# Kernel optimization log

Measured on AMD Instinct MI355X. Metric: run time of the kernel, lower is better.

## Reference

```python
import jax, jax.numpy as jnp
import numpy as np

N = 8192
NUM_CLASSES = 5
DIM = 3
EPS = 15.0
MIN_POINTS = 5
N_BATCH = 2


def setup_inputs() -> dict:
    key = jax.random.key(0)
    k1, k2, k3, k4 = jax.random.split(key, 4)
    # coords in a 96^3 box so eps=15 neighborhoods contain > minPoints same-group points
    coords = jax.random.uniform(k1, (N, DIM)) * 96.0
    batch = jax.random.randint(k2, (N, 1), 0, N_BATCH).astype(jnp.float32)
    feat = jax.random.normal(k3, (N, 1))
    seg = jax.random.normal(k4, (N, NUM_CLASSES))
    x = jnp.concatenate([coords, batch, feat, seg], axis=1).astype(jnp.float32)
    return {"x": x}


def _dbscan_labels(x):
    """Per-point DBSCAN cluster labels, run independently per (batch, class) group.
    noise = -1; cluster ids start at 0 within each group, ordered by the smallest
    point index of each cluster's core component (matches the serial scan order
    of the original implementation). Border points get the smallest adjacent
    cluster id (= first cluster to reach them in the serial algorithm)."""
    data = x[:, :-NUM_CLASSES]                 # (N, dim+2)
    seg = x[:, -NUM_CLASSES:]                  # (N, C)
    cls = jnp.argmax(seg, axis=1).astype(jnp.int32)
    b = data[:, DIM].astype(jnp.int32)
    pts = data[:, :DIM]                        # (N, 3)
    group = b * NUM_CLASSES + cls              # (N,) group id per point

    # pairwise squared distances via gram trick; d < eps  <=>  d2 < eps^2
    p2 = jnp.sum(pts * pts, axis=1)
    d2 = p2[:, None] + p2[None, :] - 2.0 * (pts @ pts.T)
    same = group[:, None] == group[None, :]
    adj = same & (d2 < EPS * EPS)              # includes self (d2 ~ 0)
    core = jnp.sum(adj, axis=1) >= MIN_POINTS  # region_query counts self too
    adjcc = adj & core[:, None] & core[None, :]

    idx = jnp.arange(N, dtype=jnp.int32)
    SENT = jnp.int32(N)
    lab0 = jnp.where(core, idx, SENT)

    # connected components of core-core graph via min-label propagation + pointer jumping
    def cond(st):
        return st[1]

    def body(st):
        lab, _ = st
        m = jnp.min(jnp.where(adjcc, lab[None, :], SENT), axis=1)
        nl = jnp.minimum(lab, m)
        safe = jnp.where(core, nl, 0)          # nl < N for core points
        nl2 = jnp.where(core, jnp.minimum(nl, nl[safe]), SENT)
        return (nl2, jnp.any(nl2 != lab))

    rep, _ = jax.lax.while_loop(cond, body, (lab0, jnp.array(True)))

    # per-group sequential cluster ids, ordered by component representative index
    is_rep = core & (rep == idx)
    cid_of_rep = jnp.zeros((N,), jnp.int32)
    for g in range(N_BATCH * NUM_CLASSES):     # fixed small count of groups
        mg = is_rep & (group == g)
        cum = jnp.cumsum(mg.astype(jnp.int32))
        cid_of_rep = jnp.where(mg, cum - 1, cid_of_rep)
    core_cid = cid_of_rep[jnp.where(core, rep, 0)]

    # border points: min cluster id among adjacent core points (same group via adj)
    nb_core = adj & core[None, :]
    BIG = jnp.int32(2 ** 30)
    bcid = jnp.min(jnp.where(nb_core, core_cid[None, :], BIG), axis=1)
    has_core_nb = jnp.any(nb_core, axis=1)
    labels = jnp.where(core, core_cid, jnp.where(has_core_nb, bcid, -1))
    return labels


def reference(x):
    labels = _dbscan_labels(x)
    data = x[:, :-NUM_CLASSES]
    # fixed-shape equivalent of the cluster gather: clustered points keep their
    # data columns (the differentiable part of the original output), noise zeroed
    clustered = jnp.where(labels[:, None] >= 0, data, 0.0)
    return labels, clustered
```

## Files before the change

### kernel.cpp

```cpp
#include <hip/hip_runtime.h>
#include <cstdint>
#include <cstddef>

#define NPTS 8192
#define NWORDS 128
#define XCOLS 10
#define MIN_PTS 5
#define NGROUPS 10
#define BIGC 0x3fffffff

#define NLCAP 1536
#define NSLICE 24
#define ECAP_S 2048
#define EACAP 8192
#define PT 1024
#define PWV 16
#define GT 1024
#define GWV 16

__global__ void __launch_bounds__(PT) k_pairs(
        const float* __restrict__ x, unsigned int* __restrict__ eAll,
        int* __restrict__ ecnt, unsigned long long* __restrict__ corebm_g,
        int* __restrict__ nlist_g, int* __restrict__ nn_g) {
    __shared__ float4 pts[NLCAP];
    __shared__ unsigned long long masks[NWORDS];
    __shared__ int pref[NWORDS];
    __shared__ int srowdeg[64];
    __shared__ int scnt, nnS;

    const int g = blockIdx.x / NSLICE;
    const int s = blockIdx.x % NSLICE;
    const int tid = threadIdx.x, lane = tid & 63, wv = tid >> 6;

    for (int k = tid; k < NLCAP; k += PT)
        pts[k] = make_float4(0.f, 0.f, 0.f, 1.0e38f);
    if (tid < 64) srowdeg[tid] = 0;
    if (tid == 0) scnt = 0;

    for (int w = wv; w < NWORDS; w += PWV) {
        int i = w * 64 + lane;
        const float2* r2 = (const float2*)(x + (size_t)i * XCOLS);
        float2 c23 = r2[1];
        float2 c45 = r2[2];
        float2 c67 = r2[3];
        float2 c89 = r2[4];
        float best = c45.y; int bc = 0;
        if (c67.x > best) { best = c67.x; bc = 1; }
        if (c67.y > best) { best = c67.y; bc = 2; }
        if (c89.x > best) { best = c89.x; bc = 3; }
        if (c89.y > best) { best = c89.y; bc = 4; }
        unsigned long long bm = __ballot((int)c23.y * 5 + bc == g);
        if (lane == 0) masks[w] = bm;
    }
    __syncthreads();
    if (wv == 0) {
        int v0 = __popcll(masks[lane]);
        int incl = v0;
        #pragma unroll
        for (int st = 1; st < 64; st <<= 1) {
            int o = __shfl_up(incl, st);
            if (lane >= st) incl += o;
        }
        pref[lane] = incl - v0;
        int tot0 = __shfl(incl, 63);
        int v1 = __popcll(masks[64 + lane]);
        int incl1 = v1;
        #pragma unroll
        for (int st = 1; st < 64; st <<= 1) {
            int o = __shfl_up(incl1, st);
            if (lane >= st) incl1 += o;
        }
        pref[64 + lane] = tot0 + incl1 - v1;
        if (lane == 63) nnS = tot0 + incl1;
    }
    __syncthreads();
    for (int w = wv; w < NWORDS; w += PWV) {
        unsigned long long bm = masks[w];
        if ((bm >> lane) & 1ull) {
            int p = pref[w] + __popcll(bm & ((1ull << lane) - 1ull));
            if (p < NLCAP) {
                int i = w * 64 + lane;
                const float2* r2 = (const float2*)(x + (size_t)i * XCOLS);
                float2 c01 = r2[0]; float2 c23 = r2[1];
                float px = c01.x, py = c01.y, pz = c23.x;
                pts[p] = make_float4(px, py, pz,
                                     0.5f * (px*px + py*py + pz*pz) - 56.25f);
                if (s == 0) nlist_g[g * NLCAP + p] = i;
            }
        }
    }
    if (s == 0 && tid == 0) nn_g[g] = (nnS > NLCAP) ? NLCAP : nnS;
    __syncthreads();
    const int NN = (nnS > NLCAP) ? NLCAP : nnS;

    const int rrow = s + NSLICE * lane;
    const float4 qu = pts[rrow];
    int rdeg = 0;
    const int NC = (NN + 31) >> 5;
    unsigned int* eg = eAll + (size_t)(g * NSLICE + s) * ECAP_S;
    for (int c = wv; c < NC; c += PWV) {
        int base = c << 5;
        unsigned int bits = 0u;
        #pragma unroll
        for (int t = 0; t < 32; t++) {
            float4 qv = pts[base + t];
            float dt = qu.x*qv.x + qu.y*qv.y + qu.z*qv.z;
            bits |= (dt > qu.w + qv.w) ? (1u << t) : 0u;
        }
        rdeg += __popc(bits);
        int d = rrow - base;
        if (d >= 31) bits = 0u;
        else if (d >= 0) bits &= ~((2u << d) - 1u);
        int cnt = __popc(bits);
        int incl = cnt;
        #pragma unroll
        for (int st = 1; st < 64; st <<= 1) {
            int o = __shfl_up(incl, st);
            if (lane >= st) incl += o;
        }
        int tot = __shfl(incl, 63);
        if (tot > 0) {
            int rb = 0;
            if (lane == 63) rb = atomicAdd(&scnt, tot);
            rb = __shfl(rb, 63);
            unsigned int p = (unsigned int)(rb + incl - cnt);
            unsigned int b = bits;
            unsigned int uhi = (unsigned int)rrow << 11;
            while (b) {
                int t = __ffs(b) - 1; b &= b - 1;
                if (p < ECAP_S) eg[p] = uhi | (unsigned int)(base + t);
                p++;
            }
        }
    }
    if (rdeg > 0) atomicAdd(&srowdeg[lane], rdeg);
    __syncthreads();
    if (wv == 0) {
        unsigned long long cb = __ballot(srowdeg[lane] >= MIN_PTS);
        if (lane == 0) {
            corebm_g[g * NSLICE + s] = cb;
            ecnt[g * NSLICE + s] = (scnt > ECAP_S) ? ECAP_S : scnt;
        }
    }
}

__global__ void __launch_bounds__(GT) k_graph(
        const unsigned int* __restrict__ eAll, const int* __restrict__ ecnt,
        const unsigned long long* __restrict__ corebm_g,
        const int* __restrict__ nlist_g, const int* __restrict__ nn_g,
        const float* __restrict__ x, float* __restrict__ out) {
    __shared__ unsigned int eA[EACAP];
    __shared__ int spar[NLCAP];
    __shared__ int scid[NLCAP];
    __shared__ int scid2[NLCAP];
    __shared__ int sbmin[NLCAP];
    __shared__ int nlist[NLCAP];
    __shared__ unsigned long long cbm[NSLICE];
    __shared__ unsigned long long corelin[NLCAP/64];
    __shared__ unsigned long long repbm[NLCAP/64];
    __shared__ int pref24[NLCAP/64];
    __shared__ int offs[NSLICE], cnts[NSLICE];
    __shared__ int NAs;

    const int g = blockIdx.x;
    const int tid = threadIdx.x, lane = tid & 63, wv = tid >> 6;
    const int NN = nn_g[g];
    volatile int* vpar = spar;

    if (wv == 0) {
        int c = 0;
        if (lane < NSLICE) {
            c = ecnt[g * NSLICE + lane];
            c = (c > ECAP_S) ? ECAP_S : c;
            cbm[lane] = corebm_g[g * NSLICE + lane];
        }
        int incl = c;
        #pragma unroll
        for (int st = 1; st < 32; st <<= 1) {
            int o = __shfl_up(incl, st);
            if (lane >= st) incl += o;
        }
        if (lane < NSLICE) { offs[lane] = incl - c; cnts[lane] = c; }
        if (lane == NSLICE - 1) NAs = incl;
    }
    for (int k = tid; k < NLCAP; k += GT) {
        spar[k] = k;
        sbmin[k] = BIGC;
        nlist[k] = nlist_g[g * NLCAP + k];
    }
    __syncthreads();
    const int NA = (NAs > EACAP) ? EACAP : NAs;
    for (int s2 = wv; s2 < NSLICE; s2 += GWV) {
        const unsigned int* eg = eAll + (size_t)(g * NSLICE + s2) * ECAP_S;
        int off = offs[s2], cn = cnts[s2];
        for (int o = lane; o < cn; o += 64) {
            int dst = off + o;
            if (dst < EACAP) eA[dst] = eg[o];
        }
    }
    for (int w = wv; w < NLCAP / 64; w += GWV) {
        int l = w * 64 + lane;
        bool b = (cbm[l % NSLICE] >> (l / NSLICE)) & 1ull;
        unsigned long long bm = __ballot(b);
        if (lane == 0) corelin[w] = bm;
    }
    __syncthreads();
    auto corebit = [&](int l) -> bool { return (corelin[l >> 6] >> (l & 63)) & 1ull; };
    auto findrep = [&](int v) -> int {
        int curr = vpar[v];
        if (curr != v) {
            int prev = v, next;
            while (curr > (next = vpar[curr])) {
                vpar[prev] = next;
                prev = curr;
                curr = next;
            }
        }
        return curr;
    };

    for (int e = tid; e < NA; e += GT) {
        unsigned int pk = eA[e];
        int u = (int)(pk >> 11), v = (int)(pk & 2047u);
        if (!(corebit(u) && corebit(v))) continue;
        int ru = findrep(u), rv = findrep(v);
        bool repeat;
        do {
            repeat = false;
            if (ru != rv) {
                int lo = (ru < rv) ? ru : rv;
                int hi = (ru < rv) ? rv : ru;
                int ret = atomicCAS(&spar[hi], hi, lo);
                if (ret != hi && ret != lo) { ru = ret; rv = lo; repeat = true; }
            }
        } while (repeat);
    }
    __syncthreads();
    for (int k = tid; k < NN; k += GT)
        spar[k] = findrep(k);
    __syncthreads();
    for (int w = wv; w < NLCAP / 64; w += GWV) {
        int l = w * 64 + lane;
        bool isr = (l < NN) && corebit(l) && (spar[l] == l);
        unsigned long long bm = __ballot(isr);
        if (lane == 0) repbm[w] = bm;
    }
    __syncthreads();
    if (wv == 0 && lane < NLCAP / 64) {
        int c = __popcll(repbm[lane]);
        int incl = c;
        #pragma unroll
        for (int st = 1; st < 32; st <<= 1) {
            int o = __shfl_up(incl, st);
            if (lane >= st) incl += o;
        }
        pref24[lane] = incl - c;
    }
    __syncthreads();
    for (int w = wv; w < NLCAP / 64; w += GWV) {
        int l = w * 64 + lane;
        unsigned long long bm = repbm[w];
        if ((bm >> lane) & 1ull)
            scid[l] = pref24[w] + __popcll(bm & ((1ull << lane) - 1ull));
    }
    __syncthreads();
    for (int k = tid; k < NLCAP; k += GT)
        scid2[k] = (k < NN && corebit(k)) ? scid[spar[k]] : BIGC;
    __syncthreads();
    for (int e = tid; e < NA; e += GT) {
        unsigned int pk = eA[e];
        int u = (int)(pk >> 11), v = (int)(pk & 2047u);
        bool cu = corebit(u), cv = corebit(v);
        if (cu == cv) continue;
        if (cu) atomicMin(&sbmin[v], scid2[u]);
        else    atomicMin(&sbmin[u], scid2[v]);
    }
    __syncthreads();
    for (int k = tid; k < NN; k += GT) {
        int i = nlist[k];
        int c = scid2[k];
        int lbl = (c != BIGC) ? c : ((sbmin[k] < BIGC) ? sbmin[k] : -1);
        out[i] = (float)lbl;
        const float* r = x + (size_t)i * XCOLS;
        float* o = out + NPTS + (size_t)i * 5;
        bool keep = lbl >= 0;
        #pragma unroll
        for (int c5 = 0; c5 < 5; c5++) o[c5] = keep ? r[c5] : 0.0f;
    }
}

extern "C" void kernel_launch(void* const* d_in, const int* in_sizes, int n_in,
                              void* d_out, int out_size, void* d_ws, size_t ws_size,
                              hipStream_t stream) {
    const float* x = (const float*)d_in[0];
    float* out = (float*)d_out;
    char* ws = (char*)d_ws;

    unsigned int* eAll       = (unsigned int*)(ws);
    int* ecnt                = (int*)(ws + 1966080);
    unsigned long long* cbm  = (unsigned long long*)(ws + 1967104);
    int* nlist_g             = (int*)(ws + 1969024);
    int* nn_g                = (int*)(ws + 2030464);

    k_pairs<<<NGROUPS * NSLICE, PT, 0, stream>>>(x, eAll, ecnt, cbm, nlist_g, nn_g);
    k_graph<<<NGROUPS, GT, 0, stream>>>(eAll, ecnt, cbm, nlist_g, nn_g, x, out);
}
```

Before: 81.00 us.

## Fuse pair and graph kernels into one launch with flag-based inter-block handoff

Merges the neighbour-pair kernel and the union-find graph kernel into a single launch. The graph blocks spin on per-slice release/acquire flags, written as a value and its complement, instead of waiting on a kernel boundary. Edge output offsets now come from a buffered two-pass per-wave prefix sum instead of a shared atomic counter. The representative-ID scan is also collapsed into a single-wave sequential pass. This removes a launch gap and atomic contention, but adds spin-waiting blocks and a dependence on co-residency. Flags persist across calls in the workspace, so stale values could be accepted before the current data is written.

```diff
diff --git a/kernel.cpp b/kernel.cpp
--- a/kernel.cpp
+++ b/kernel.cpp
@@ -13,31 +13,43 @@
 #define NSLICE 24
 #define ECAP_S 2048
 #define EACAP 8192
-#define PT 1024
-#define PWV 16
-#define GT 1024
-#define GWV 16
-
-__global__ void __launch_bounds__(PT) k_pairs(
-        const float* __restrict__ x, unsigned int* __restrict__ eAll,
-        int* __restrict__ ecnt, unsigned long long* __restrict__ corebm_g,
-        int* __restrict__ nlist_g, int* __restrict__ nn_g) {
-    __shared__ float4 pts[NLCAP];
-    __shared__ unsigned long long masks[NWORDS];
-    __shared__ int pref[NWORDS];
-    __shared__ int srowdeg[64];
-    __shared__ int scnt, nnS;
-
-    const int g = blockIdx.x / NSLICE;
-    const int s = blockIdx.x % NSLICE;
+#define NCMAX (NLCAP / 32)
+#define NT 1024
+#define NWV 16
+
+struct SmemP {
+    float4 pts[NLCAP];
+    unsigned long long masks[NWORDS];
+    int pref[NWORDS];
+    unsigned int bitsbuf[NCMAX * 64];
+    int wave_tot[NWV], wave_off[NWV];
+    int srowdeg[64];
+    int nnS, totE;
+};
+struct SmemG {
+    unsigned int eA[EACAP];
+    int spar[NLCAP];
+    int scid[NLCAP];
+    int scid2[NLCAP];
+    int sbmin[NLCAP];
+    int nlist[NLCAP];
+    unsigned long long cbm[NSLICE];
+    unsigned long long corelin[NLCAP / 64];
+    int offs[NSLICE], cnts[NSLICE];
+    int NAs;
+};
+
+__device__ __forceinline__ void do_pairs(const float* __restrict__ x, int g, int s,
+        SmemP& sm, unsigned int* __restrict__ eAll, unsigned int* __restrict__ flags,
+        unsigned long long* __restrict__ corebm_g, int* __restrict__ nlist_g,
+        int* __restrict__ nn_g) {
     const int tid = threadIdx.x, lane = tid & 63, wv = tid >> 6;
 
-    for (int k = tid; k < NLCAP; k += PT)
-        pts[k] = make_float4(0.f, 0.f, 0.f, 1.0e38f);
-    if (tid < 64) srowdeg[tid] = 0;
-    if (tid == 0) scnt = 0;
-
-    for (int w = wv; w < NWORDS; w += PWV) {
+    for (int k = tid; k < NLCAP; k += NT)
+        sm.pts[k] = make_float4(0.f, 0.f, 0.f, 1.0e38f);
+    if (tid < 64) sm.srowdeg[tid] = 0;
+
+    for (int w = wv; w < NWORDS; w += NWV) {
         int i = w * 64 + lane;
         const float2* r2 = (const float2*)(x + (size_t)i * XCOLS);
         float2 c23 = r2[1];
@@ -50,60 +62,59 @@
         if (c89.x > best) { best = c89.x; bc = 3; }
         if (c89.y > best) { best = c89.y; bc = 4; }
         unsigned long long bm = __ballot((int)c23.y * 5 + bc == g);
-        if (lane == 0) masks[w] = bm;
+        if (lane == 0) sm.masks[w] = bm;
     }
     __syncthreads();
     if (wv == 0) {
-        int v0 = __popcll(masks[lane]);
+        int v0 = __popcll(sm.masks[lane]);
         int incl = v0;
         #pragma unroll
         for (int st = 1; st < 64; st <<= 1) {
             int o = __shfl_up(incl, st);
             if (lane >= st) incl += o;
         }
-        pref[lane] = incl - v0;
+        sm.pref[lane] = incl - v0;
         int tot0 = __shfl(incl, 63);
-        int v1 = __popcll(masks[64 + lane]);
+        int v1 = __popcll(sm.masks[64 + lane]);
         int incl1 = v1;
         #pragma unroll
         for (int st = 1; st < 64; st <<= 1) {
             int o = __shfl_up(incl1, st);
             if (lane >= st) incl1 += o;
         }
-        pref[64 + lane] = tot0 + incl1 - v1;
-        if (lane == 63) nnS = tot0 + incl1;
-    }
-    __syncthreads();
-    for (int w = wv; w < NWORDS; w += PWV) {
-        unsigned long long bm = masks[w];
+        sm.pref[64 + lane] = tot0 + incl1 - v1;
+        if (lane == 63) sm.nnS = tot0 + incl1;
+    }
+    __syncthreads();
+    for (int w = wv; w < NWORDS; w += NWV) {
+        unsigned long long bm = sm.masks[w];
         if ((bm >> lane) & 1ull) {
-            int p = pref[w] + __popcll(bm & ((1ull << lane) - 1ull));
+            int p = sm.pref[w] + __popcll(bm & ((1ull << lane) - 1ull));
             if (p < NLCAP) {
                 int i = w * 64 + lane;
                 const float2* r2 = (const float2*)(x + (size_t)i * XCOLS);
                 float2 c01 = r2[0]; float2 c23 = r2[1];
                 float px = c01.x, py = c01.y, pz = c23.x;
-                pts[p] = make_float4(px, py, pz,
-                                     0.5f * (px*px + py*py + pz*pz) - 56.25f);
+                sm.pts[p] = make_float4(px, py, pz,
+                                        0.5f * (px*px + py*py + pz*pz) - 56.25f);
                 if (s == 0) nlist_g[g * NLCAP + p] = i;
             }
         }
     }
-    if (s == 0 && tid == 0) nn_g[g] = (nnS > NLCAP) ? NLCAP : nnS;
-    __syncthreads();
-    const int NN = (nnS > NLCAP) ? NLCAP : nnS;
+    if (s == 0 && tid == 0) nn_g[g] = (sm.nnS > NLCAP) ? NLCAP : sm.nnS;
+    __syncthreads();
+    const int NN = (sm.nnS > NLCAP) ? NLCAP : sm.nnS;
 
     const int rrow = s + NSLICE * lane;
-    const float4 qu = pts[rrow];
-    int rdeg = 0;
+    const float4 qu = sm.pts[rrow];
+    int rdeg = 0, wcnt = 0;
     const int NC = (NN + 31) >> 5;
-    unsigned int* eg = eAll + (size_t)(g * NSLICE + s) * ECAP_S;
-    for (int c = wv; c < NC; c += PWV) {
+    for (int c = wv; c < NC; c += NWV) {
         int base = c << 5;
         unsigned int bits = 0u;
         #pragma unroll
         for (int t = 0; t < 32; t++) {
-            float4 qv = pts[base + t];
+            float4 qv = sm.pts[base + t];
             float dt = qu.x*qv.x + qu.y*qv.y + qu.z*qv.z;
             bits |= (dt > qu.w + qv.w) ? (1u << t) : 0u;
         }
@@ -111,6 +122,30 @@
         int d = rrow - base;
         if (d >= 31) bits = 0u;
         else if (d >= 0) bits &= ~((2u << d) - 1u);
+        sm.bitsbuf[c * 64 + lane] = bits;
+        wcnt += __popc(bits);
+    }
+    #pragma unroll
+    for (int st = 32; st >= 1; st >>= 1) wcnt += __shfl_xor(wcnt, st);
+    if (lane == 0) sm.wave_tot[wv] = wcnt;
+    if (rdeg > 0) atomicAdd(&sm.srowdeg[lane], rdeg);
+    __syncthreads();
+    if (wv == 0 && lane < NWV) {
+        int v = sm.wave_tot[lane];
+        int incl = v;
+        #pragma unroll
+        for (int st = 1; st < NWV; st <<= 1) {
+            int o = __shfl_up(incl, st);
+            if (lane >= st) incl += o;
+        }
+        sm.wave_off[lane] = incl - v;
+        if (lane == NWV - 1) sm.totE = incl;
+    }
+    __syncthreads();
+    unsigned int* eg = eAll + (size_t)(g * NSLICE + s) * ECAP_S;
+    unsigned int running = (unsigned int)sm.wave_off[wv];
+    for (int c = wv; c < NC; c += NWV) {
+        unsigned int bits = sm.bitsbuf[c * 64 + lane];
         int cnt = __popc(bits);
         int incl = cnt;
         #pragma unroll
@@ -120,59 +155,60 @@
         }
         int tot = __shfl(incl, 63);
         if (tot > 0) {
-            int rb = 0;
-            if (lane == 63) rb = atomicAdd(&scnt, tot);
-            rb = __shfl(rb, 63);
-            unsigned int p = (unsigned int)(rb + incl - cnt);
+            unsigned int p = running + (unsigned int)(incl - cnt);
             unsigned int b = bits;
             unsigned int uhi = (unsigned int)rrow << 11;
+            int base = c << 5;
             while (b) {
                 int t = __ffs(b) - 1; b &= b - 1;
                 if (p < ECAP_S) eg[p] = uhi | (unsigned int)(base + t);
                 p++;
             }
         }
-    }
-    if (rdeg > 0) atomicAdd(&srowdeg[lane], rdeg);
-    __syncthreads();
-    if (wv == 0) {
-        unsigned long long cb = __ballot(srowdeg[lane] >= MIN_PTS);
-        if (lane == 0) {
-            corebm_g[g * NSLICE + s] = cb;
-            ecnt[g * NSLICE + s] = (scnt > ECAP_S) ? ECAP_S : scnt;
-        }
+        running += (unsigned int)tot;
+    }
+    __syncthreads();
+    unsigned long long cb = 0;
+    if (wv == 0) cb = __ballot(sm.srowdeg[lane] >= MIN_PTS);
+    __threadfence();
+    __syncthreads();
+    if (tid == 0) {
+        corebm_g[g * NSLICE + s] = cb;
+        int tE = sm.totE; if (tE > ECAP_S) tE = ECAP_S;
+        __threadfence();
+        __hip_atomic_store(&flags[2 * (g * NSLICE + s)],     (unsigned int)tE,
+                           __ATOMIC_RELEASE, __HIP_MEMORY_SCOPE_AGENT);
+        __hip_atomic_store(&flags[2 * (g * NSLICE + s) + 1], ~(unsigned int)tE,
+                           __ATOMIC_RELEASE, __HIP_MEMORY_SCOPE_AGENT);
     }
 }
 
-__global__ void __launch_bounds__(GT) k_graph(
-        const unsigned int* __restrict__ eAll, const int* __restrict__ ecnt,
+__device__ __forceinline__ void do_graph(const float* __restrict__ x, int g,
+        SmemG& sm, const unsigned int* __restrict__ eAll, unsigned int* __restrict__ flags,
         const unsigned long long* __restrict__ corebm_g,
         const int* __restrict__ nlist_g, const int* __restrict__ nn_g,
-        const float* __restrict__ x, float* __restrict__ out) {
-    __shared__ unsigned int eA[EACAP];
-    __shared__ int spar[NLCAP];
-    __shared__ int scid[NLCAP];
-    __shared__ int scid2[NLCAP];
-    __shared__ int sbmin[NLCAP];
-    __shared__ int nlist[NLCAP];
-    __shared__ unsigned long long cbm[NSLICE];
-    __shared__ unsigned long long corelin[NLCAP/64];
-    __shared__ unsigned long long repbm[NLCAP/64];
-    __shared__ int pref24[NLCAP/64];
-    __shared__ int offs[NSLICE], cnts[NSLICE];
-    __shared__ int NAs;
-
-    const int g = blockIdx.x;
+        float* __restrict__ out) {
     const int tid = threadIdx.x, lane = tid & 63, wv = tid >> 6;
-    const int NN = nn_g[g];
-    volatile int* vpar = spar;
+    volatile int* vpar = sm.spar;
 
     if (wv == 0) {
+        bool valid = (lane >= NSLICE);
+        unsigned int f0v = 0;
+        while (!__all(valid)) {
+            if (!valid) {
+                unsigned int a = __hip_atomic_load(&flags[2 * (g * NSLICE + lane)],
+                                    __ATOMIC_ACQUIRE, __HIP_MEMORY_SCOPE_AGENT);
+                unsigned int b = __hip_atomic_load(&flags[2 * (g * NSLICE + lane) + 1],
+                                    __ATOMIC_ACQUIRE, __HIP_MEMORY_SCOPE_AGENT);
+                if (a == ~b) { valid = true; f0v = a; }
+            }
+            if (!__all(valid)) __builtin_amdgcn_s_sleep(2);
+        }
         int c = 0;
         if (lane < NSLICE) {
-            c = ecnt[g * NSLICE + lane];
-            c = (c > ECAP_S) ? ECAP_S : c;
-            cbm[lane] = corebm_g[g * NSLICE + lane];
+            c = (f0v > ECAP_S) ? ECAP_S : (int)f0v;
+            sm.cnts[lane] = c;
+            sm.cbm[lane] = corebm_g[g * NSLICE + lane];
         }
         int incl = c;
         #pragma unroll
@@ -180,32 +216,31 @@
             int o = __shfl_up(incl, st);
             if (lane >= st) incl += o;
         }
-        if (lane < NSLICE) { offs[lane] = incl - c; cnts[lane] = c; }
-        if (lane == NSLICE - 1) NAs = incl;
-    }
-    for (int k = tid; k < NLCAP; k += GT) {
-        spar[k] = k;
-        sbmin[k] = BIGC;
-        nlist[k] = nlist_g[g * NLCAP + k];
-    }
-    __syncthreads();
-    const int NA = (NAs > EACAP) ? EACAP : NAs;
-    for (int s2 = wv; s2 < NSLICE; s2 += GWV) {
+        if (lane < NSLICE) sm.offs[lane] = incl - c;
+        if (lane == NSLICE - 1) sm.NAs = incl;
+    }
+    for (int k = tid; k < NLCAP; k += NT) { sm.spar[k] = k; sm.sbmin[k] = BIGC; }
+    __syncthreads();
+    const int NN = nn_g[g];
+    const int NA = (sm.NAs > EACAP) ? EACAP : sm.NAs;
+
+    for (int k = tid; k < NLCAP; k += NT) sm.nlist[k] = nlist_g[g * NLCAP + k];
+    for (int s2 = wv; s2 < NSLICE; s2 += NWV) {
         const unsigned int* eg = eAll + (size_t)(g * NSLICE + s2) * ECAP_S;
-        int off = offs[s2], cn = cnts[s2];
+        int off = sm.offs[s2], cn = sm.cnts[s2];
         for (int o = lane; o < cn; o += 64) {
             int dst = off + o;
-            if (dst < EACAP) eA[dst] = eg[o];
-        }
-    }
-    for (int w = wv; w < NLCAP / 64; w += GWV) {
+            if (dst < EACAP) sm.eA[dst] = eg[o];
+        }
+    }
+    for (int w = wv; w < NLCAP / 64; w += NWV) {
         int l = w * 64 + lane;
-        bool b = (cbm[l % NSLICE] >> (l / NSLICE)) & 1ull;
-        unsigned long long bm = __ballot(b);
-        if (lane == 0) corelin[w] = bm;
-    }
-    __syncthreads();
-    auto corebit = [&](int l) -> bool { return (corelin[l >> 6] >> (l & 63)) & 1ull; };
+        bool bb = (sm.cbm[l % NSLICE] >> (l / NSLICE)) & 1ull;
+        unsigned long long bm = __ballot(bb);
+        if (lane == 0) sm.corelin[w] = bm;
+    }
+    __syncthreads();
+    auto corebit = [&](int l) -> bool { return (sm.corelin[l >> 6] >> (l & 63)) & 1ull; };
     auto findrep = [&](int v) -> int {
         int curr = vpar[v];
         if (curr != v) {
@@ -219,8 +254,8 @@
         return curr;
     };
 
-    for (int e = tid; e < NA; e += GT) {
-        unsigned int pk = eA[e];
+    for (int e = tid; e < NA; e += NT) {
+        unsigned int pk = sm.eA[e];
         int u = (int)(pk >> 11), v = (int)(pk & 2047u);
         if (!(corebit(u) && corebit(v))) continue;
         int ru = findrep(u), rv = findrep(v);
@@ -230,62 +265,64 @@
             if (ru != rv) {
                 int lo = (ru < rv) ? ru : rv;
                 int hi = (ru < rv) ? rv : ru;
-                int ret = atomicCAS(&spar[hi], hi, lo);
+                int ret = atomicCAS(&sm.spar[hi], hi, lo);
                 if (ret != hi && ret != lo) { ru = ret; rv = lo; repeat = true; }
             }
         } while (repeat);
     }
     __syncthreads();
-    for (int k = tid; k < NN; k += GT)
-        spar[k] = findrep(k);
-    __syncthreads();
-    for (int w = wv; w < NLCAP / 64; w += GWV) {
-        int l = w * 64 + lane;
-        bool isr = (l < NN) && corebit(l) && (spar[l] == l);
-        unsigned long long bm = __ballot(isr);
-        if (lane == 0) repbm[w] = bm;
-    }
-    __syncthreads();
-    if (wv == 0 && lane < NLCAP / 64) {
-        int c = __popcll(repbm[lane]);
-        int incl = c;
-        #pragma unroll
-        for (int st = 1; st < 32; st <<= 1) {
-            int o = __shfl_up(incl, st);
-            if (lane >= st) incl += o;
-        }
-        pref24[lane] = incl - c;
-    }
-    __syncthreads();
-    for (int w = wv; w < NLCAP / 64; w += GWV) {
-        int l = w * 64 + lane;
-        unsigned long long bm = repbm[w];
-        if ((bm >> lane) & 1ull)
-            scid[l] = pref24[w] + __popcll(bm & ((1ull << lane) - 1ull));
-    }
-    __syncthreads();
-    for (int k = tid; k < NLCAP; k += GT)
-        scid2[k] = (k < NN && corebit(k)) ? scid[spar[k]] : BIGC;
-    __syncthreads();
-    for (int e = tid; e < NA; e += GT) {
-        unsigned int pk = eA[e];
+    for (int k = tid; k < NN; k += NT)
+        sm.spar[k] = findrep(k);
+    __syncthreads();
+    if (wv == 0) {
+        int runcnt = 0;
+        for (int w = 0; w < NLCAP / 64; w++) {
+            int l = w * 64 + lane;
+            bool isr = (l < NN) && corebit(l) && (sm.spar[l] == l);
+            unsigned long long bm = __ballot(isr);
+            if (isr) sm.scid[l] = runcnt + __popcll(bm & ((1ull << lane) - 1ull));
+            runcnt += __popcll(bm);
+        }
+    }
+    __syncthreads();
+    for (int k = tid; k < NLCAP; k += NT)
+        sm.scid2[k] = (k < NN && corebit(k)) ? sm.scid[sm.spar[k]] : BIGC;
+    __syncthreads();
+    for (int e = tid; e < NA; e += NT) {
+        unsigned int pk = sm.eA[e];
         int u = (int)(pk >> 11), v = (int)(pk & 2047u);
         bool cu = corebit(u), cv = corebit(v);
         if (cu == cv) continue;
-        if (cu) atomicMin(&sbmin[v], scid2[u]);
-        else    atomicMin(&sbmin[u], scid2[v]);
-    }
-    __syncthreads();
-    for (int k = tid; k < NN; k += GT) {
-        int i = nlist[k];
-        int c = scid2[k];
-        int lbl = (c != BIGC) ? c : ((sbmin[k] < BIGC) ? sbmin[k] : -1);
+        if (cu) atomicMin(&sm.sbmin[v], sm.scid2[u]);
+        else    atomicMin(&sm.sbmin[u], sm.scid2[v]);
+    }
+    __syncthreads();
+    for (int k = tid; k < NN; k += NT) {
+        int i = sm.nlist[k];
+        int c = sm.scid2[k];
+        int lbl = (c != BIGC) ? c : ((sm.sbmin[k] < BIGC) ? sm.sbmin[k] : -1);
         out[i] = (float)lbl;
         const float* r = x + (size_t)i * XCOLS;
         float* o = out + NPTS + (size_t)i * 5;
         bool keep = lbl >= 0;
         #pragma unroll
         for (int c5 = 0; c5 < 5; c5++) o[c5] = keep ? r[c5] : 0.0f;
+    }
+}
+
+__global__ void __launch_bounds__(NT) k_all(const float* __restrict__ x,
+        float* __restrict__ out, unsigned int* __restrict__ eAll,
+        unsigned int* __restrict__ flags, unsigned long long* __restrict__ corebm_g,
+        int* __restrict__ nlist_g, int* __restrict__ nn_g) {
+    __shared__ __align__(16) char smem[
+        sizeof(SmemG) > sizeof(SmemP) ? sizeof(SmemG) : sizeof(SmemP)];
+    const int b = blockIdx.x;
+    if (b < NGROUPS * NSLICE) {
+        do_pairs(x, b / NSLICE, b % NSLICE, *reinterpret_cast<SmemP*>(smem),
+                 eAll, flags, corebm_g, nlist_g, nn_g);
+    } else {
+        do_graph(x, b - NGROUPS * NSLICE, *reinterpret_cast<SmemG*>(smem),
+                 eAll, flags, corebm_g, nlist_g, nn_g, out);
     }
 }
 
@@ -297,11 +334,11 @@
     char* ws = (char*)d_ws;
 
     unsigned int* eAll       = (unsigned int*)(ws);
-    int* ecnt                = (int*)(ws + 1966080);
-    unsigned long long* cbm  = (unsigned long long*)(ws + 1967104);
-    int* nlist_g             = (int*)(ws + 1969024);
-    int* nn_g                = (int*)(ws + 2030464);
-
-    k_pairs<<<NGROUPS * NSLICE, PT, 0, stream>>>(x, eAll, ecnt, cbm, nlist_g, nn_g);
-    k_graph<<<NGROUPS, GT, 0, stream>>>(eAll, ecnt, cbm, nlist_g, nn_g, x, out);
+    unsigned int* flags      = (unsigned int*)(ws + 1966080);
+    unsigned long long* cbm  = (unsigned long long*)(ws + 1968128);
+    int* nlist_g             = (int*)(ws + 1970048);
+    int* nn_g                = (int*)(ws + 2031488);
+
+    k_all<<<NGROUPS * NSLICE + NGROUPS, NT, 0, stream>>>(x, out, eAll, flags,
+                                                         cbm, nlist_g, nn_g);
 }
```

After: 150.0 us. +85.2%, slower.

## Fuse edge staging with union-find and collapse cluster-id numbering into one wave

Applied to the files above, without the earlier changes.

The union-find merge now runs directly on edges as they are loaded from global memory into shared memory, which removes a barrier and a second pass over the shared edge array. The four-step rep-bitmap, prefix and scid scheme is replaced by a single-wave sequential ballot scan, and the scid2 and nlist shared arrays are dropped in favour of indirect lookups. This cuts barriers and shared-memory footprint, but puts the rep numbering on one wave serially and adds an indirection per border edge.

```diff
diff --git a/kernel.cpp b/kernel.cpp
--- a/kernel.cpp
+++ b/kernel.cpp
@@ -152,13 +152,9 @@
     __shared__ unsigned int eA[EACAP];
     __shared__ int spar[NLCAP];
     __shared__ int scid[NLCAP];
-    __shared__ int scid2[NLCAP];
     __shared__ int sbmin[NLCAP];
-    __shared__ int nlist[NLCAP];
     __shared__ unsigned long long cbm[NSLICE];
     __shared__ unsigned long long corelin[NLCAP/64];
-    __shared__ unsigned long long repbm[NLCAP/64];
-    __shared__ int pref24[NLCAP/64];
     __shared__ int offs[NSLICE], cnts[NSLICE];
     __shared__ int NAs;
 
@@ -172,6 +168,7 @@
         if (lane < NSLICE) {
             c = ecnt[g * NSLICE + lane];
             c = (c > ECAP_S) ? ECAP_S : c;
+            cnts[lane] = c;
             cbm[lane] = corebm_g[g * NSLICE + lane];
         }
         int incl = c;
@@ -180,24 +177,14 @@
             int o = __shfl_up(incl, st);
             if (lane >= st) incl += o;
         }
-        if (lane < NSLICE) { offs[lane] = incl - c; cnts[lane] = c; }
+        if (lane < NSLICE) offs[lane] = incl - c;
         if (lane == NSLICE - 1) NAs = incl;
     }
     for (int k = tid; k < NLCAP; k += GT) {
         spar[k] = k;
         sbmin[k] = BIGC;
-        nlist[k] = nlist_g[g * NLCAP + k];
-    }
-    __syncthreads();
-    const int NA = (NAs > EACAP) ? EACAP : NAs;
-    for (int s2 = wv; s2 < NSLICE; s2 += GWV) {
-        const unsigned int* eg = eAll + (size_t)(g * NSLICE + s2) * ECAP_S;
-        int off = offs[s2], cn = cnts[s2];
-        for (int o = lane; o < cn; o += 64) {
-            int dst = off + o;
-            if (dst < EACAP) eA[dst] = eg[o];
-        }
-    }
+    }
+    __syncthreads();
     for (int w = wv; w < NLCAP / 64; w += GWV) {
         int l = w * 64 + lane;
         bool b = (cbm[l % NSLICE] >> (l / NSLICE)) & 1ull;
@@ -219,67 +206,58 @@
         return curr;
     };
 
-    for (int e = tid; e < NA; e += GT) {
-        unsigned int pk = eA[e];
-        int u = (int)(pk >> 11), v = (int)(pk & 2047u);
-        if (!(corebit(u) && corebit(v))) continue;
-        int ru = findrep(u), rv = findrep(v);
-        bool repeat;
-        do {
-            repeat = false;
-            if (ru != rv) {
-                int lo = (ru < rv) ? ru : rv;
-                int hi = (ru < rv) ? rv : ru;
-                int ret = atomicCAS(&spar[hi], hi, lo);
-                if (ret != hi && ret != lo) { ru = ret; rv = lo; repeat = true; }
-            }
-        } while (repeat);
+    const int NA = (NAs > EACAP) ? EACAP : NAs;
+    for (int s2 = wv; s2 < NSLICE; s2 += GWV) {
+        const unsigned int* eg = eAll + (size_t)(g * NSLICE + s2) * ECAP_S;
+        int off = offs[s2], cn = cnts[s2];
+        for (int o = lane; o < cn; o += 64) {
+            unsigned int pk = eg[o];
+            int dst = off + o;
+            if (dst < EACAP) eA[dst] = pk;
+            int u = (int)(pk >> 11), v = (int)(pk & 2047u);
+            if (!(corebit(u) && corebit(v))) continue;
+            int ru = findrep(u), rv = findrep(v);
+            bool repeat;
+            do {
+                repeat = false;
+                if (ru != rv) {
+                    int lo = (ru < rv) ? ru : rv;
+                    int hi = (ru < rv) ? rv : ru;
+                    int ret = atomicCAS(&spar[hi], hi, lo);
+                    if (ret != hi && ret != lo) { ru = ret; rv = lo; repeat = true; }
+                }
+            } while (repeat);
+        }
     }
     __syncthreads();
     for (int k = tid; k < NN; k += GT)
         spar[k] = findrep(k);
     __syncthreads();
-    for (int w = wv; w < NLCAP / 64; w += GWV) {
-        int l = w * 64 + lane;
-        bool isr = (l < NN) && corebit(l) && (spar[l] == l);
-        unsigned long long bm = __ballot(isr);
-        if (lane == 0) repbm[w] = bm;
-    }
-    __syncthreads();
-    if (wv == 0 && lane < NLCAP / 64) {
-        int c = __popcll(repbm[lane]);
-        int incl = c;
-        #pragma unroll
-        for (int st = 1; st < 32; st <<= 1) {
-            int o = __shfl_up(incl, st);
-            if (lane >= st) incl += o;
-        }
-        pref24[lane] = incl - c;
-    }
-    __syncthreads();
-    for (int w = wv; w < NLCAP / 64; w += GWV) {
-        int l = w * 64 + lane;
-        unsigned long long bm = repbm[w];
-        if ((bm >> lane) & 1ull)
-            scid[l] = pref24[w] + __popcll(bm & ((1ull << lane) - 1ull));
-    }
-    __syncthreads();
-    for (int k = tid; k < NLCAP; k += GT)
-        scid2[k] = (k < NN && corebit(k)) ? scid[spar[k]] : BIGC;
+    if (wv == 0) {
+        int runcnt = 0;
+        for (int w = 0; w < NLCAP / 64; w++) {
+            int l = w * 64 + lane;
+            bool isr = (l < NN) && corebit(l) && (spar[l] == l);
+            unsigned long long bm = __ballot(isr);
+            if (isr) scid[l] = runcnt + __popcll(bm & ((1ull << lane) - 1ull));
+            runcnt += __popcll(bm);
+        }
+    }
     __syncthreads();
     for (int e = tid; e < NA; e += GT) {
         unsigned int pk = eA[e];
         int u = (int)(pk >> 11), v = (int)(pk & 2047u);
         bool cu = corebit(u), cv = corebit(v);
         if (cu == cv) continue;
-        if (cu) atomicMin(&sbmin[v], scid2[u]);
-        else    atomicMin(&sbmin[u], scid2[v]);
+        if (cu) atomicMin(&sbmin[v], scid[spar[u]]);
+        else    atomicMin(&sbmin[u], scid[spar[v]]);
     }
     __syncthreads();
     for (int k = tid; k < NN; k += GT) {
-        int i = nlist[k];
-        int c = scid2[k];
-        int lbl = (c != BIGC) ? c : ((sbmin[k] < BIGC) ? sbmin[k] : -1);
+        int i = nlist_g[g * NLCAP + k];
+        int lbl;
+        if (corebit(k))      lbl = scid[spar[k]];
+        else                 lbl = (sbmin[k] < BIGC) ? sbmin[k] : -1;
         out[i] = (float)lbl;
         const float* r = x + (size_t)i * XCOLS;
         float* o = out + NPTS + (size_t)i * 5;
```

Result: no change. 82.07 us (+1.3%).
